# Optimization experiments

Measured on AMD Instinct MI355X. Metric: run time of the kernel, lower is better.

Reference implementation:

```python
import jax, jax.numpy as jnp
import numpy as np

B, T, C = 4, 2048, 768
H, D = 12, 64          # num_heads, head_size
R = 64                 # kv_lora_rank
ROPE_THETA = 10000.0


def setup_inputs() -> dict:
    key = jax.random.key(0)
    ks = jax.random.split(key, 8)
    s = lambda fan_in: 1.0 / np.sqrt(fan_in)
    return {
        "x":      jax.random.normal(ks[0], (B, T, C), jnp.float32),
        "Wq":     jax.random.normal(ks[1], (C, H * D), jnp.float32) * s(C),
        "Wdown":  jax.random.normal(ks[2], (C, R), jnp.float32) * s(C),
        "ln_g":   jnp.ones((R,), jnp.float32),
        "ln_b":   jnp.zeros((R,), jnp.float32),
        "Wup":    jax.random.normal(ks[3], (R, 2 * H * D), jnp.float32) * s(R),
        "Wo":     jax.random.normal(ks[4], (H * D, C), jnp.float32) * s(H * D),
        "bo":     jnp.zeros((C,), jnp.float32),
    }


def _rope_cos_sin(t, d, dtype):
    # freqs over half-dim, repeated twice (rotate-half convention)
    inv_freq = 1.0 / (ROPE_THETA ** (jnp.arange(0, d, 2, dtype=jnp.float32) / d))
    ang = jnp.arange(t, dtype=jnp.float32)[:, None] * inv_freq[None, :]  # [T, D/2]
    ang = jnp.concatenate([ang, ang], axis=-1)                            # [T, D]
    return jnp.cos(ang).astype(dtype), jnp.sin(ang).astype(dtype)


def _apply_rope(q, cos, sin):
    # q: [B, H, T, D]; cos/sin: [T, D]
    d2 = q.shape[-1] // 2
    rot = jnp.concatenate([-q[..., d2:], q[..., :d2]], axis=-1)
    return q * cos + rot * sin


def reference(x, Wq, Wdown, ln_g, ln_b, Wup, Wo, bo):
    b, t, c = x.shape
    q = (x @ Wq).reshape(b, t, H, D).transpose(0, 2, 1, 3)  # [B,H,T,D]

    ckv = x @ Wdown                                         # [B,T,R]
    mu = jnp.mean(ckv, axis=-1, keepdims=True)
    var = jnp.var(ckv, axis=-1, keepdims=True)
    ckv = (ckv - mu) * jax.lax.rsqrt(var + 1e-5) * ln_g + ln_b

    kv = (ckv @ Wup).reshape(b, t, 2, H, D)
    k = kv[:, :, 0].transpose(0, 2, 1, 3)                   # [B,H,T,D]
    v = kv[:, :, 1].transpose(0, 2, 1, 3)

    cos, sin = _rope_cos_sin(t, D, x.dtype)
    q = _apply_rope(q, cos, sin)
    k = _apply_rope(k, cos, sin)

    wei = jnp.einsum("bhqd,bhkd->bhqk", q, k) * (D ** -0.5)
    causal = jnp.tril(jnp.ones((t, t), bool))
    wei = jnp.where(causal, wei, -jnp.inf)
    wei = jax.nn.softmax(wei, axis=-1)                      # dropout: eval mode (identity)

    out = jnp.einsum("bhqk,bhkd->bhqd", wei, v)             # [B,H,T,D]
    out = out.transpose(0, 2, 1, 3).reshape(b, t, H * D)
    return out @ Wo + bo
```

## Files before the change

kernel.cpp:

```cpp
#include <hip/hip_runtime.h>
#include <hip/hip_bf16.h>
#include <math.h>

#define B_ 4
#define T_ 2048
#define C_ 768
#define H_ 12
#define D_ 64
#define R_ 64
#define BT_ (B_*T_)
#define HD_ (H_*D_)

typedef __attribute__((ext_vector_type(8))) short bf16x8;
typedef __attribute__((ext_vector_type(4))) float f32x4;

__device__ inline short f2bf(float f) {
  union { float f; unsigned u; } x; x.f = f;
  unsigned r = x.u + 0x7fffu + ((x.u >> 16) & 1u);
  return (short)(r >> 16);
}
__device__ inline float bf2f(short s) {
  union { unsigned u; float f; } x; x.u = ((unsigned)(unsigned short)s) << 16;
  return x.f;
}
__device__ inline unsigned pk_bf16(float a, float b) {
#if __has_builtin(__builtin_amdgcn_cvt_pk_bf16_f32)
  auto t = __builtin_amdgcn_cvt_pk_bf16_f32(a, b);
  unsigned u; __builtin_memcpy(&u, &t, sizeof(unsigned)); return u;
#else
  union { float f; unsigned u; } x, y; x.f = a; y.f = b;
  unsigned ra = (x.u + 0x7fffu + ((x.u >> 16) & 1u)) >> 16;
  unsigned rb = (y.u + 0x7fffu + ((y.u >> 16) & 1u)) & 0xffff0000u;
  return ra | rb;
#endif
}
__device__ inline float fexp2(float x) {
#if __has_builtin(__builtin_amdgcn_exp2f)
  return __builtin_amdgcn_exp2f(x);
#else
  return exp2f(x);
#endif
}
typedef __attribute__((address_space(3))) unsigned lds_u32;
typedef __attribute__((address_space(1))) const unsigned glb_u32;
__device__ inline void gload_lds16(const void* g, void* l) {
  __builtin_amdgcn_global_load_lds((glb_u32*)g, (lds_u32*)l, 16, 0, 0);
}

__global__ void convert_f32_bf16(const float* __restrict__ in, short* __restrict__ out, int n4) {
  int i = blockIdx.x * blockDim.x + threadIdx.x;
  if (i < n4) {
    float4 v = ((const float4*)in)[i];
    short4 o;
    o.x = f2bf(v.x); o.y = f2bf(v.y); o.z = f2bf(v.z); o.w = f2bf(v.w);
    ((short4*)out)[i] = o;
  }
}

__global__ void transpose_all(const float* __restrict__ Wq, const float* __restrict__ Wd,
                              const float* __restrict__ Wup, const float* __restrict__ Wo,
                              short* __restrict__ W1T, short* __restrict__ WupT,
                              short* __restrict__ WoT) {
  int idx = blockIdx.x * blockDim.x + threadIdx.x;
  const int S1 = 768*768, S2 = 64*768, S3 = 1536*64, S4 = 768*768;
  if (idx < S1) {
    int n = idx / 768, k = idx - n*768;
    W1T[idx] = f2bf(Wq[(size_t)k*768 + n]);
  } else if (idx < S1+S2) {
    int i = idx - S1; int n = i / 768, k = i - n*768;
    W1T[idx] = f2bf(Wd[(size_t)k*64 + n]);
  } else if (idx < S1+S2+S3) {
    int i = idx - S1 - S2; int n = i / 64, k = i - n*64;
    WupT[i] = f2bf(Wup[(size_t)k*1536 + n]);
  } else if (idx < S1+S2+S3+S4) {
    int i = idx - S1 - S2 - S3; int n = i / 768, k = i - n*768;
    WoT[i] = f2bf(Wo[(size_t)k*768 + n]);
  }
}

__global__ void rope_tab(float* __restrict__ cs, float* __restrict__ sn) {
  int idx = blockIdx.x * blockDim.x + threadIdx.x;
  if (idx >= T_ * 32) return;
  int j = idx & 31, t = idx >> 5;
  float invf = exp2f(-(float)j * (13.287712379549449f / 32.f));
  float a = (float)t * invf;
  cs[idx] = cosf(a);
  sn[idx] = sinf(a);
}

template<int MODE>
__global__ __launch_bounds__(256) void gemm128(
    const short* __restrict__ A, const short* __restrict__ Bt,
    int M, int N, int K, int NBvalid,
    float* __restrict__ out0, const float* __restrict__ bias,
    short* __restrict__ ob0, short* __restrict__ ob1,
    const float* __restrict__ cs, const float* __restrict__ sn)
{
  __shared__ short As[128 * 64];
  __shared__ short Bs[128 * 64];
  const int m0 = blockIdx.x * 128;
  const int n0 = blockIdx.y * 128;
  const int tid = threadIdx.x, lane = tid & 63, w = tid >> 6;
  const int wr = w >> 1, wc = w & 1;
  const int fr = lane & 15, fk = (lane >> 4) * 8;
  const int rstage = lane >> 3;
  const int cstage = (lane & 7) * 8;

  f32x4 acc[4][4] = {};

  for (int k0 = 0; k0 < K; k0 += 64) {
    __syncthreads();
    #pragma unroll
    for (int i = 0; i < 4; ++i) {
      int c = w * 4 + i;
      int r = c * 8 + rstage;
      gload_lds16(&A[(size_t)(m0 + r) * K + k0 + cstage], &As[c * 512]);
      if (n0 + c * 8 < NBvalid)
        gload_lds16(&Bt[(size_t)(n0 + r) * K + k0 + cstage], &Bs[c * 512]);
    }
    __syncthreads();
    #pragma unroll
    for (int kk = 0; kk < 64; kk += 32) {
      bf16x8 a[4], b[4];
      #pragma unroll
      for (int i = 0; i < 4; ++i) {
        a[i] = *(const bf16x8*)&As[(wr * 64 + i * 16 + fr) * 64 + kk + fk];
        b[i] = *(const bf16x8*)&Bs[(wc * 64 + i * 16 + fr) * 64 + kk + fk];
      }
      #pragma unroll
      for (int mi = 0; mi < 4; ++mi)
        #pragma unroll
        for (int ni = 0; ni < 4; ++ni)
          acc[mi][ni] = __builtin_amdgcn_mfma_f32_16x16x32_bf16(a[mi], b[ni], acc[mi][ni], 0, 0, 0);
    }
  }

  const int er = (lane >> 4) * 4, ec = lane & 15;
  const int colbase = n0 + wc * 64;

  if constexpr (MODE == 2) {
    #pragma unroll
    for (int mi = 0; mi < 4; ++mi)
      #pragma unroll
      for (int r = 0; r < 4; ++r) {
        int row = m0 + wr * 64 + mi * 16 + er + r;
        #pragma unroll
        for (int ni = 0; ni < 4; ++ni) {
          int col = colbase + ni * 16 + ec;
          out0[(size_t)row * N + col] = acc[mi][ni][r] + bias[col];
        }
      }
    return;
  }

  if (colbase < 768) {
    int h = colbase >> 6;
    #pragma unroll
    for (int mi = 0; mi < 4; ++mi)
      #pragma unroll
      for (int r = 0; r < 4; ++r) {
        int row = m0 + wr * 64 + mi * 16 + er + r;
        int t = row & (T_ - 1), bb = row >> 11;
        short* dst = ob0 + (((size_t)(bb * H_ + h)) * T_ + t) * 64;
        #pragma unroll
        for (int ni = 0; ni < 2; ++ni) {
          int d = ni * 16 + ec;
          float c = cs[t * 32 + d], s = sn[t * 32 + d];
          float x0 = acc[mi][ni][r], x1 = acc[mi][ni + 2][r];
          dst[d]      = f2bf(x0 * c - x1 * s);
          dst[d + 32] = f2bf(x1 * c + x0 * s);
        }
      }
  } else if constexpr (MODE == 0) {
    if (colbase < 832) {
      #pragma unroll
      for (int mi = 0; mi < 4; ++mi)
        #pragma unroll
        for (int r = 0; r < 4; ++r) {
          int row = m0 + wr * 64 + mi * 16 + er + r;
          #pragma unroll
          for (int ni = 0; ni < 4; ++ni)
            ob1[(size_t)row * 64 + ni * 16 + ec] = f2bf(acc[mi][ni][r]);
        }
    }
  } else {
    int h = (colbase - 768) >> 6;
    #pragma unroll
    for (int mi = 0; mi < 4; ++mi) {
      int row0 = m0 + wr * 64 + mi * 16 + er;
      int t = row0 & (T_ - 1), bb = row0 >> 11;
      #pragma unroll
      for (int ni = 0; ni < 4; ++ni) {
        int dd = ni * 16 + ec;
        short4 s4;
        s4.x = f2bf(acc[mi][ni][0]); s4.y = f2bf(acc[mi][ni][1]);
        s4.z = f2bf(acc[mi][ni][2]); s4.w = f2bf(acc[mi][ni][3]);
        *(short4*)&ob1[((size_t)(bb * H_ + h) * 64 + dd) * T_ + t] = s4;
      }
    }
  }
}

__global__ __launch_bounds__(256) void ln_rows(const short* __restrict__ raw,
                                               short* __restrict__ outb,
                                               const float* __restrict__ g,
                                               const float* __restrict__ bta) {
  int row = blockIdx.x * 4 + (threadIdx.x >> 6);
  int lane = threadIdx.x & 63;
  float v = bf2f(raw[(size_t)row * 64 + lane]);
  float s = v, s2 = v * v;
  #pragma unroll
  for (int off = 1; off < 64; off <<= 1) {
    s += __shfl_xor(s, off);
    s2 += __shfl_xor(s2, off);
  }
  float mu = s * (1.f/64.f);
  float var = s2 * (1.f/64.f) - mu * mu;
  float rstd = rsqrtf(var + 1e-5f);
  outb[(size_t)row * 64 + lane] = f2bf((v - mu) * rstd * g[lane] + bta[lane]);
}

#define SC2_ 0.18033688f

__global__ __launch_bounds__(256, 4) void attn_mfma(
    const short* __restrict__ qgl, const short* __restrict__ kg,
    const short* __restrict__ vtg, short* __restrict__ o)
{
  __shared__ short Ks[8 * 512];
  __shared__ short Vts[8 * 512];
  __shared__ short Ps[4 * 32 * 72];

  const int bh = blockIdx.x;
  const int qt = 15 - blockIdx.y;
  const int tid = threadIdx.x, lane = tid & 63, w = tid >> 6;
  const int q16 = lane & 15, quad = lane >> 4;
  const int q0 = qt * 128;
  const int qw = q0 + w * 32;
  short* Pw = &Ps[w * 32 * 72];

  bf16x8 bq[2][2];
  #pragma unroll
  for (int qg = 0; qg < 2; ++qg) {
    const short* qrow = qgl + ((size_t)bh * T_ + qw + qg * 16 + q16) * 64;
    bq[qg][0] = *(const bf16x8*)&qrow[quad * 8];
    bq[qg][1] = *(const bf16x8*)&qrow[32 + quad * 8];
  }
  f32x4 oacc[2][4] = {};
  float lrun[2] = {0.f, 0.f};
  const short* kb  = kg  + (size_t)bh * T_ * 64;
  const short* vtb = vtg + (size_t)bh * 64 * T_;
  const int ktmax = q0 + 64;

  for (int kt = 0; kt <= ktmax; kt += 64) {
    __syncthreads();
    #pragma unroll
    for (int i = 0; i < 2; ++i) {
      int c = w * 2 + i;
      int s = c >> 1, ch = c & 1;
      gload_lds16(kb  + (size_t)(kt + s * 16 + q16) * 64 + ch * 32 + quad * 8, &Ks[c * 512]);
      gload_lds16(vtb + (size_t)(s * 16 + q16) * T_ + kt + ch * 32 + quad * 8, &Vts[c * 512]);
    }
    __syncthreads();

    #pragma unroll
    for (int qg = 0; qg < 2; ++qg) {
      const int qbase = qw + qg * 16;
      if (kt > qbase + 15) continue;
      const bool part = (kt + 63 > qbase);
      float ls = 0.f;
      #pragma unroll
      for (int s = 0; s < 4; ++s) {
        bf16x8 a0 = *(const bf16x8*)&Ks[(s * 2 + 0) * 512 + lane * 8];
        bf16x8 a1 = *(const bf16x8*)&Ks[(s * 2 + 1) * 512 + lane * 8];
        f32x4 t0 = {};
        t0 = __builtin_amdgcn_mfma_f32_16x16x32_bf16(a0, bq[qg][0], t0, 0, 0, 0);
        t0 = __builtin_amdgcn_mfma_f32_16x16x32_bf16(a1, bq[qg][1], t0, 0, 0, 0);
        float pv[4];
        if (!part) {
          #pragma unroll
          for (int r = 0; r < 4; ++r) pv[r] = fexp2(t0[r] * SC2_);
        } else {
          #pragma unroll
          for (int r = 0; r < 4; ++r) {
            int key = kt + s * 16 + quad * 4 + r;
            pv[r] = (key <= qbase + q16) ? fexp2(t0[r] * SC2_) : 0.f;
          }
        }
        ls += (pv[0] + pv[1]) + (pv[2] + pv[3]);
        uint2 uu;
        uu.x = pk_bf16(pv[0], pv[1]);
        uu.y = pk_bf16(pv[2], pv[3]);
        *(uint2*)&Pw[(qg * 16 + q16) * 72 + s * 16 + quad * 4] = uu;
      }
      ls += __shfl_xor(ls, 16);
      ls += __shfl_xor(ls, 32);
      lrun[qg] += ls;

      #pragma unroll
      for (int c = 0; c < 2; ++c) {
        bf16x8 bp = *(const bf16x8*)&Pw[(qg * 16 + q16) * 72 + c * 32 + quad * 8];
        #pragma unroll
        for (int ms = 0; ms < 4; ++ms) {
          bf16x8 av = *(const bf16x8*)&Vts[(ms * 2 + c) * 512 + lane * 8];
          oacc[qg][ms] = __builtin_amdgcn_mfma_f32_16x16x32_bf16(av, bp, oacc[qg][ms], 0, 0, 0);
        }
      }
    }
  }

  int b = bh / H_, h = bh - b * H_;
  #pragma unroll
  for (int qg = 0; qg < 2; ++qg) {
    float inv = 1.f / lrun[qg];
    #pragma unroll
    for (int ms = 0; ms < 4; ++ms) {
      uint2 uu;
      uu.x = pk_bf16(oacc[qg][ms][0] * inv, oacc[qg][ms][1] * inv);
      uu.y = pk_bf16(oacc[qg][ms][2] * inv, oacc[qg][ms][3] * inv);
      *(uint2*)&Pw[(qg * 16 + q16) * 72 + ms * 16 + quad * 4] = uu;
    }
    int row = lane >> 2, cc2 = (lane & 3) * 16;
    uint4 r0 = *(const uint4*)&Pw[(qg * 16 + row) * 72 + cc2];
    uint4 r1 = *(const uint4*)&Pw[(qg * 16 + row) * 72 + cc2 + 8];
    int t = qw + qg * 16 + row;
    short* orow = o + ((size_t)(b * T_ + t)) * HD_ + h * 64 + cc2;
    *(uint4*)&orow[0] = r0;
    *(uint4*)&orow[8] = r1;
  }
}

extern "C" void kernel_launch(void* const* d_in, const int* in_sizes, int n_in,
                              void* d_out, int out_size, void* d_ws, size_t ws_size,
                              hipStream_t stream) {
  (void)in_sizes; (void)n_in; (void)out_size; (void)ws_size;
  const float* x     = (const float*)d_in[0];
  const float* Wq    = (const float*)d_in[1];
  const float* Wdown = (const float*)d_in[2];
  const float* ln_g  = (const float*)d_in[3];
  const float* ln_b  = (const float*)d_in[4];
  const float* Wup   = (const float*)d_in[5];
  const float* Wo    = (const float*)d_in[6];
  const float* bo    = (const float*)d_in[7];
  float* out = (float*)d_out;

  char* w = (char*)d_ws;
  short* x_bf   = (short*)w;  w += (size_t)BT_ * C_    * 2;
  short* W1T    = (short*)w;  w += (size_t)832 * C_    * 2;
  short* WupT   = (short*)w;  w += (size_t)2*HD_ * R_  * 2;
  short* WoT    = (short*)w;  w += (size_t)HD_ * C_    * 2;
  short* ckvraw = (short*)w;  w += (size_t)BT_ * R_    * 2;
  short* ckv    = (short*)w;  w += (size_t)BT_ * R_    * 2;
  short* qb     = (short*)w;  w += (size_t)BT_ * HD_   * 2;
  short* kb     = (short*)w;  w += (size_t)BT_ * HD_   * 2;
  short* vt     = (short*)w;  w += (size_t)BT_ * HD_   * 2;
  short* att    = (short*)w;  w += (size_t)BT_ * HD_   * 2;
  float* cs_t   = (float*)w;  w += (size_t)T_ * 32 * 4;
  float* sn_t   = (float*)w;  w += (size_t)T_ * 32 * 4;

  rope_tab<<<(T_*32 + 255)/256, 256, 0, stream>>>(cs_t, sn_t);
  convert_f32_bf16<<<(BT_*C_/4 + 255)/256, 256, 0, stream>>>(x, x_bf, BT_*C_/4);
  {
    const int tot = 768*768 + 64*768 + 1536*64 + 768*768;
    transpose_all<<<(tot + 255)/256, 256, 0, stream>>>(Wq, Wdown, Wup, Wo, W1T, WupT, WoT);
  }

  gemm128<0><<<dim3(BT_/128, 7), 256, 0, stream>>>(
      x_bf, W1T, BT_, 896, C_, 832, nullptr, nullptr, qb, ckvraw, cs_t, sn_t);

  ln_rows<<<BT_/4, 256, 0, stream>>>(ckvraw, ckv, ln_g, ln_b);

  gemm128<1><<<dim3(BT_/128, 12), 256, 0, stream>>>(
      ckv, WupT, BT_, 2*HD_, R_, 2*HD_, nullptr, nullptr, kb, vt, cs_t, sn_t);

  attn_mfma<<<dim3(B_*H_, T_/128), 256, 0, stream>>>(qb, kb, vt, att);

  gemm128<2><<<dim3(BT_/128, 6), 256, 0, stream>>>(
      att, WoT, BT_, C_, HD_, C_, out, bo, nullptr, nullptr, nullptr, nullptr);
}
```

Measured before the change: 230.3 us.

## Fuse LayerNorm into GEMM epilogue, merge prep kernels, rebalance causal attention tiles

Folds the rope table computation into the weight transpose kernel and fuses the latent LayerNorm into the first GEMM's epilogue, which removes two launches and the round trip through the raw ckv buffer. The V-transpose epilogue now stages through LDS so that global stores are coalesced 16-byte rows. The attention kernel now uses 64-row query tiles with one 16-row group per wave. Each block processes a late tile and its mirrored early tile, balancing causal work across blocks, and the occupancy launch-bound hint is dropped. In exchange, each attention block does more sequential work and has fewer rows per wave to reuse each K/V load.

```diff
diff --git a/kernel.cpp b/kernel.cpp
--- a/kernel.cpp
+++ b/kernel.cpp
@@ -57,12 +57,13 @@
   }
 }
 
-__global__ void transpose_all(const float* __restrict__ Wq, const float* __restrict__ Wd,
-                              const float* __restrict__ Wup, const float* __restrict__ Wo,
-                              short* __restrict__ W1T, short* __restrict__ WupT,
-                              short* __restrict__ WoT) {
+__global__ void prep_all(const float* __restrict__ Wq, const float* __restrict__ Wd,
+                         const float* __restrict__ Wup, const float* __restrict__ Wo,
+                         short* __restrict__ W1T, short* __restrict__ WupT,
+                         short* __restrict__ WoT,
+                         float* __restrict__ cs, float* __restrict__ sn) {
   int idx = blockIdx.x * blockDim.x + threadIdx.x;
-  const int S1 = 768*768, S2 = 64*768, S3 = 1536*64, S4 = 768*768;
+  const int S1 = 768*768, S2 = 64*768, S3 = 1536*64, S4 = 768*768, S5 = T_*32;
   if (idx < S1) {
     int n = idx / 768, k = idx - n*768;
     W1T[idx] = f2bf(Wq[(size_t)k*768 + n]);
@@ -75,17 +76,14 @@
   } else if (idx < S1+S2+S3+S4) {
     int i = idx - S1 - S2 - S3; int n = i / 768, k = i - n*768;
     WoT[i] = f2bf(Wo[(size_t)k*768 + n]);
-  }
-}
-
-__global__ void rope_tab(float* __restrict__ cs, float* __restrict__ sn) {
-  int idx = blockIdx.x * blockDim.x + threadIdx.x;
-  if (idx >= T_ * 32) return;
-  int j = idx & 31, t = idx >> 5;
-  float invf = exp2f(-(float)j * (13.287712379549449f / 32.f));
-  float a = (float)t * invf;
-  cs[idx] = cosf(a);
-  sn[idx] = sinf(a);
+  } else if (idx < S1+S2+S3+S4+S5) {
+    int i = idx - S1 - S2 - S3 - S4;
+    int j = i & 31, t = i >> 5;
+    float invf = exp2f(-(float)j * (13.287712379549449f / 32.f));
+    float a = (float)t * invf;
+    cs[i] = cosf(a);
+    sn[i] = sinf(a);
+  }
 }
 
 template<int MODE>
@@ -93,6 +91,7 @@
     const short* __restrict__ A, const short* __restrict__ Bt,
     int M, int N, int K, int NBvalid,
     float* __restrict__ out0, const float* __restrict__ bias,
+    const float* __restrict__ bias2,
     short* __restrict__ ob0, short* __restrict__ ob1,
     const float* __restrict__ cs, const float* __restrict__ sn)
 {
@@ -153,176 +152,209 @@
     return;
   }
 
-  if (colbase < 768) {
-    int h = colbase >> 6;
-    #pragma unroll
-    for (int mi = 0; mi < 4; ++mi)
-      #pragma unroll
-      for (int r = 0; r < 4; ++r) {
-        int row = m0 + wr * 64 + mi * 16 + er + r;
-        int t = row & (T_ - 1), bb = row >> 11;
-        short* dst = ob0 + (((size_t)(bb * H_ + h)) * T_ + t) * 64;
-        #pragma unroll
-        for (int ni = 0; ni < 2; ++ni) {
-          int d = ni * 16 + ec;
-          float c = cs[t * 32 + d], s = sn[t * 32 + d];
-          float x0 = acc[mi][ni][r], x1 = acc[mi][ni + 2][r];
-          dst[d]      = f2bf(x0 * c - x1 * s);
-          dst[d + 32] = f2bf(x1 * c + x0 * s);
-        }
-      }
-  } else if constexpr (MODE == 0) {
-    if (colbase < 832) {
+  if constexpr (MODE == 0) {
+    if (colbase < 768) {
+      int h = colbase >> 6;
       #pragma unroll
       for (int mi = 0; mi < 4; ++mi)
         #pragma unroll
         for (int r = 0; r < 4; ++r) {
           int row = m0 + wr * 64 + mi * 16 + er + r;
-          #pragma unroll
-          for (int ni = 0; ni < 4; ++ni)
-            ob1[(size_t)row * 64 + ni * 16 + ec] = f2bf(acc[mi][ni][r]);
+          int t = row & (T_ - 1), bb = row >> 11;
+          short* dst = ob0 + (((size_t)(bb * H_ + h)) * T_ + t) * 64;
+          #pragma unroll
+          for (int ni = 0; ni < 2; ++ni) {
+            int d = ni * 16 + ec;
+            float c = cs[t * 32 + d], s = sn[t * 32 + d];
+            float x0 = acc[mi][ni][r], x1 = acc[mi][ni + 2][r];
+            dst[d]      = f2bf(x0 * c - x1 * s);
+            dst[d + 32] = f2bf(x1 * c + x0 * s);
+          }
+        }
+    } else if (colbase < 832) {
+      #pragma unroll
+      for (int mi = 0; mi < 4; ++mi)
+        #pragma unroll
+        for (int r = 0; r < 4; ++r) {
+          float s = 0.f, s2 = 0.f;
+          #pragma unroll
+          for (int ni = 0; ni < 4; ++ni) { float v = acc[mi][ni][r]; s += v; s2 += v*v; }
+          #pragma unroll
+          for (int off = 1; off < 16; off <<= 1) {
+            s  += __shfl_xor(s, off);
+            s2 += __shfl_xor(s2, off);
+          }
+          float mu = s * (1.f/64.f);
+          float var = s2 * (1.f/64.f) - mu * mu;
+          float rstd = rsqrtf(var + 1e-5f);
+          int row = m0 + wr * 64 + mi * 16 + er + r;
+          #pragma unroll
+          for (int ni = 0; ni < 4; ++ni) {
+            int d = ni * 16 + ec;
+            ob1[(size_t)row * 64 + d] = f2bf((acc[mi][ni][r] - mu) * rstd * bias[d] + bias2[d]);
+          }
         }
     }
   } else {
-    int h = (colbase - 768) >> 6;
-    #pragma unroll
-    for (int mi = 0; mi < 4; ++mi) {
-      int row0 = m0 + wr * 64 + mi * 16 + er;
-      int t = row0 & (T_ - 1), bb = row0 >> 11;
-      #pragma unroll
-      for (int ni = 0; ni < 4; ++ni) {
-        int dd = ni * 16 + ec;
-        short4 s4;
-        s4.x = f2bf(acc[mi][ni][0]); s4.y = f2bf(acc[mi][ni][1]);
-        s4.z = f2bf(acc[mi][ni][2]); s4.w = f2bf(acc[mi][ni][3]);
-        *(short4*)&ob1[((size_t)(bb * H_ + h) * 64 + dd) * T_ + t] = s4;
-      }
-    }
-  }
-}
-
-__global__ __launch_bounds__(256) void ln_rows(const short* __restrict__ raw,
-                                               short* __restrict__ outb,
-                                               const float* __restrict__ g,
-                                               const float* __restrict__ bta) {
-  int row = blockIdx.x * 4 + (threadIdx.x >> 6);
-  int lane = threadIdx.x & 63;
-  float v = bf2f(raw[(size_t)row * 64 + lane]);
-  float s = v, s2 = v * v;
-  #pragma unroll
-  for (int off = 1; off < 64; off <<= 1) {
-    s += __shfl_xor(s, off);
-    s2 += __shfl_xor(s2, off);
-  }
-  float mu = s * (1.f/64.f);
-  float var = s2 * (1.f/64.f) - mu * mu;
-  float rstd = rsqrtf(var + 1e-5f);
-  outb[(size_t)row * 64 + lane] = f2bf((v - mu) * rstd * g[lane] + bta[lane]);
+    if (colbase < 768) {
+      int h = colbase >> 6;
+      #pragma unroll
+      for (int mi = 0; mi < 4; ++mi)
+        #pragma unroll
+        for (int r = 0; r < 4; ++r) {
+          int row = m0 + wr * 64 + mi * 16 + er + r;
+          int t = row & (T_ - 1), bb = row >> 11;
+          short* dst = ob0 + (((size_t)(bb * H_ + h)) * T_ + t) * 64;
+          #pragma unroll
+          for (int ni = 0; ni < 2; ++ni) {
+            int d = ni * 16 + ec;
+            float c = cs[t * 32 + d], s = sn[t * 32 + d];
+            float x0 = acc[mi][ni][r], x1 = acc[mi][ni + 2][r];
+            dst[d]      = f2bf(x0 * c - x1 * s);
+            dst[d + 32] = f2bf(x1 * c + x0 * s);
+          }
+        }
+    } else {
+      __syncthreads();
+      short* Wl = (w < 2) ? &As[w * 4096] : &Bs[(w - 2) * 4096];
+      int h = (colbase - 768) >> 6;
+      #pragma unroll
+      for (int mi = 0; mi < 4; ++mi) {
+        int tl0 = mi * 16 + er;
+        #pragma unroll
+        for (int ni = 0; ni < 4; ++ni) {
+          int d = ni * 16 + ec;
+          int col = (tl0 + (d & 7) * 8) & 63;
+          uint2 uu;
+          uu.x = pk_bf16(acc[mi][ni][0], acc[mi][ni][1]);
+          uu.y = pk_bf16(acc[mi][ni][2], acc[mi][ni][3]);
+          *(uint2*)&Wl[d * 64 + col] = uu;
+        }
+      }
+      __syncthreads();
+      int bb = m0 >> 11;
+      int tg0 = (m0 & (T_ - 1)) + wr * 64;
+      int dlow = lane >> 3, tc = lane & 7;
+      #pragma unroll
+      for (int j = 0; j < 8; ++j) {
+        int d = j * 8 + dlow;
+        int col = (tc * 8 + (d & 7) * 8) & 63;
+        uint4 vv = *(const uint4*)&Wl[d * 64 + col];
+        *(uint4*)&ob1[((size_t)(bb * H_ + h) * 64 + d) * T_ + tg0 + tc * 8] = vv;
+      }
+    }
+  }
 }
 
 #define SC2_ 0.18033688f
 
-__global__ __launch_bounds__(256, 4) void attn_mfma(
+__global__ __launch_bounds__(256) void attn_mfma(
     const short* __restrict__ qgl, const short* __restrict__ kg,
     const short* __restrict__ vtg, short* __restrict__ o)
 {
   __shared__ short Ks[8 * 512];
   __shared__ short Vts[8 * 512];
-  __shared__ short Ps[4 * 32 * 72];
+  __shared__ short Ps[4 * 16 * 72];
 
   const int bh = blockIdx.x;
-  const int qt = 15 - blockIdx.y;
   const int tid = threadIdx.x, lane = tid & 63, w = tid >> 6;
   const int q16 = lane & 15, quad = lane >> 4;
-  const int q0 = qt * 128;
-  const int qw = q0 + w * 32;
-  short* Pw = &Ps[w * 32 * 72];
-
-  bf16x8 bq[2][2];
-  #pragma unroll
-  for (int qg = 0; qg < 2; ++qg) {
-    const short* qrow = qgl + ((size_t)bh * T_ + qw + qg * 16 + q16) * 64;
-    bq[qg][0] = *(const bf16x8*)&qrow[quad * 8];
-    bq[qg][1] = *(const bf16x8*)&qrow[32 + quad * 8];
-  }
-  f32x4 oacc[2][4] = {};
-  float lrun[2] = {0.f, 0.f};
+  short* Pw = &Ps[w * 16 * 72];
   const short* kb  = kg  + (size_t)bh * T_ * 64;
   const short* vtb = vtg + (size_t)bh * 64 * T_;
-  const int ktmax = q0 + 64;
-
-  for (int kt = 0; kt <= ktmax; kt += 64) {
-    __syncthreads();
-    #pragma unroll
-    for (int i = 0; i < 2; ++i) {
-      int c = w * 2 + i;
-      int s = c >> 1, ch = c & 1;
-      gload_lds16(kb  + (size_t)(kt + s * 16 + q16) * 64 + ch * 32 + quad * 8, &Ks[c * 512]);
-      gload_lds16(vtb + (size_t)(s * 16 + q16) * T_ + kt + ch * 32 + quad * 8, &Vts[c * 512]);
-    }
-    __syncthreads();
-
-    #pragma unroll
-    for (int qg = 0; qg < 2; ++qg) {
-      const int qbase = qw + qg * 16;
-      if (kt > qbase + 15) continue;
-      const bool part = (kt + 63 > qbase);
-      float ls = 0.f;
+  const int b = bh / H_, h = bh - b * H_;
+
+  #pragma unroll
+  for (int phase = 0; phase < 2; ++phase) {
+    const int qt = phase == 0 ? (31 - (int)blockIdx.y) : (int)blockIdx.y;
+    const int q0 = qt * 64 + w * 16;
+    const int qidx = q0 + q16;
+
+    const short* qrow = qgl + ((size_t)bh * T_ + qidx) * 64;
+    bf16x8 bq0 = *(const bf16x8*)&qrow[quad * 8];
+    bf16x8 bq1 = *(const bf16x8*)&qrow[32 + quad * 8];
+
+    f32x4 oacc[4] = {};
+    float lrun = 0.f;
+    const int qlast = qt * 64;
+
+    for (int kt = 0; kt <= qlast; kt += 64) {
+      __syncthreads();
+      #pragma unroll
+      for (int i = 0; i < 2; ++i) {
+        int c = w * 2 + i;
+        int s = c >> 1, ch = c & 1;
+        gload_lds16(kb  + (size_t)(kt + s * 16 + q16) * 64 + ch * 32 + quad * 8, &Ks[c * 512]);
+        gload_lds16(vtb + (size_t)(s * 16 + q16) * T_ + kt + ch * 32 + quad * 8, &Vts[c * 512]);
+      }
+      __syncthreads();
+
+      f32x4 sacc[4];
       #pragma unroll
       for (int s = 0; s < 4; ++s) {
         bf16x8 a0 = *(const bf16x8*)&Ks[(s * 2 + 0) * 512 + lane * 8];
         bf16x8 a1 = *(const bf16x8*)&Ks[(s * 2 + 1) * 512 + lane * 8];
         f32x4 t0 = {};
-        t0 = __builtin_amdgcn_mfma_f32_16x16x32_bf16(a0, bq[qg][0], t0, 0, 0, 0);
-        t0 = __builtin_amdgcn_mfma_f32_16x16x32_bf16(a1, bq[qg][1], t0, 0, 0, 0);
-        float pv[4];
-        if (!part) {
-          #pragma unroll
-          for (int r = 0; r < 4; ++r) pv[r] = fexp2(t0[r] * SC2_);
-        } else {
+        t0 = __builtin_amdgcn_mfma_f32_16x16x32_bf16(a0, bq0, t0, 0, 0, 0);
+        t0 = __builtin_amdgcn_mfma_f32_16x16x32_bf16(a1, bq1, t0, 0, 0, 0);
+        sacc[s] = t0;
+      }
+
+      float pv[16];
+      float ls = 0.f;
+      if (kt != qlast) {
+        #pragma unroll
+        for (int s = 0; s < 4; ++s)
+          #pragma unroll
+          for (int r = 0; r < 4; ++r) {
+            float p = fexp2(sacc[s][r] * SC2_);
+            pv[s * 4 + r] = p; ls += p;
+          }
+      } else {
+        #pragma unroll
+        for (int s = 0; s < 4; ++s)
           #pragma unroll
           for (int r = 0; r < 4; ++r) {
             int key = kt + s * 16 + quad * 4 + r;
-            pv[r] = (key <= qbase + q16) ? fexp2(t0[r] * SC2_) : 0.f;
-          }
-        }
-        ls += (pv[0] + pv[1]) + (pv[2] + pv[3]);
-        uint2 uu;
-        uu.x = pk_bf16(pv[0], pv[1]);
-        uu.y = pk_bf16(pv[2], pv[3]);
-        *(uint2*)&Pw[(qg * 16 + q16) * 72 + s * 16 + quad * 4] = uu;
+            float p = (key <= qidx) ? fexp2(sacc[s][r] * SC2_) : 0.f;
+            pv[s * 4 + r] = p; ls += p;
+          }
       }
       ls += __shfl_xor(ls, 16);
       ls += __shfl_xor(ls, 32);
-      lrun[qg] += ls;
+      lrun += ls;
+
+      #pragma unroll
+      for (int s = 0; s < 4; ++s) {
+        uint2 uu;
+        uu.x = pk_bf16(pv[s * 4 + 0], pv[s * 4 + 1]);
+        uu.y = pk_bf16(pv[s * 4 + 2], pv[s * 4 + 3]);
+        *(uint2*)&Pw[q16 * 72 + s * 16 + quad * 4] = uu;
+      }
 
       #pragma unroll
       for (int c = 0; c < 2; ++c) {
-        bf16x8 bp = *(const bf16x8*)&Pw[(qg * 16 + q16) * 72 + c * 32 + quad * 8];
+        bf16x8 bp = *(const bf16x8*)&Pw[q16 * 72 + c * 32 + quad * 8];
         #pragma unroll
         for (int ms = 0; ms < 4; ++ms) {
           bf16x8 av = *(const bf16x8*)&Vts[(ms * 2 + c) * 512 + lane * 8];
-          oacc[qg][ms] = __builtin_amdgcn_mfma_f32_16x16x32_bf16(av, bp, oacc[qg][ms], 0, 0, 0);
-        }
-      }
-    }
-  }
-
-  int b = bh / H_, h = bh - b * H_;
-  #pragma unroll
-  for (int qg = 0; qg < 2; ++qg) {
-    float inv = 1.f / lrun[qg];
+          oacc[ms] = __builtin_amdgcn_mfma_f32_16x16x32_bf16(av, bp, oacc[ms], 0, 0, 0);
+        }
+      }
+    }
+
+    float inv = 1.f / lrun;
     #pragma unroll
     for (int ms = 0; ms < 4; ++ms) {
       uint2 uu;
-      uu.x = pk_bf16(oacc[qg][ms][0] * inv, oacc[qg][ms][1] * inv);
-      uu.y = pk_bf16(oacc[qg][ms][2] * inv, oacc[qg][ms][3] * inv);
-      *(uint2*)&Pw[(qg * 16 + q16) * 72 + ms * 16 + quad * 4] = uu;
+      uu.x = pk_bf16(oacc[ms][0] * inv, oacc[ms][1] * inv);
+      uu.y = pk_bf16(oacc[ms][2] * inv, oacc[ms][3] * inv);
+      *(uint2*)&Pw[q16 * 72 + ms * 16 + quad * 4] = uu;
     }
     int row = lane >> 2, cc2 = (lane & 3) * 16;
-    uint4 r0 = *(const uint4*)&Pw[(qg * 16 + row) * 72 + cc2];
-    uint4 r1 = *(const uint4*)&Pw[(qg * 16 + row) * 72 + cc2 + 8];
-    int t = qw + qg * 16 + row;
+    uint4 r0 = *(const uint4*)&Pw[row * 72 + cc2];
+    uint4 r1 = *(const uint4*)&Pw[row * 72 + cc2 + 8];
+    int t = q0 + row;
     short* orow = o + ((size_t)(b * T_ + t)) * HD_ + h * 64 + cc2;
     *(uint4*)&orow[0] = r0;
     *(uint4*)&orow[8] = r1;
@@ -348,7 +380,6 @@
   short* W1T    = (short*)w;  w += (size_t)832 * C_    * 2;
   short* WupT   = (short*)w;  w += (size_t)2*HD_ * R_  * 2;
   short* WoT    = (short*)w;  w += (size_t)HD_ * C_    * 2;
-  short* ckvraw = (short*)w;  w += (size_t)BT_ * R_    * 2;
   short* ckv    = (short*)w;  w += (size_t)BT_ * R_    * 2;
   short* qb     = (short*)w;  w += (size_t)BT_ * HD_   * 2;
   short* kb     = (short*)w;  w += (size_t)BT_ * HD_   * 2;
@@ -357,23 +388,20 @@
   float* cs_t   = (float*)w;  w += (size_t)T_ * 32 * 4;
   float* sn_t   = (float*)w;  w += (size_t)T_ * 32 * 4;
 
-  rope_tab<<<(T_*32 + 255)/256, 256, 0, stream>>>(cs_t, sn_t);
+  {
+    const int tot = 768*768 + 64*768 + 1536*64 + 768*768 + T_*32;
+    prep_all<<<(tot + 255)/256, 256, 0, stream>>>(Wq, Wdown, Wup, Wo, W1T, WupT, WoT, cs_t, sn_t);
+  }
   convert_f32_bf16<<<(BT_*C_/4 + 255)/256, 256, 0, stream>>>(x, x_bf, BT_*C_/4);
-  {
-    const int tot = 768*768 + 64*768 + 1536*64 + 768*768;
-    transpose_all<<<(tot + 255)/256, 256, 0, stream>>>(Wq, Wdown, Wup, Wo, W1T, WupT, WoT);
-  }
 
   gemm128<0><<<dim3(BT_/128, 7), 256, 0, stream>>>(
-      x_bf, W1T, BT_, 896, C_, 832, nullptr, nullptr, qb, ckvraw, cs_t, sn_t);
-
-  ln_rows<<<BT_/4, 256, 0, stream>>>(ckvraw, ckv, ln_g, ln_b);
+      x_bf, W1T, BT_, 896, C_, 832, nullptr, ln_g, ln_b, qb, ckv, cs_t, sn_t);
 
   gemm128<1><<<dim3(BT_/128, 12), 256, 0, stream>>>(
-      ckv, WupT, BT_, 2*HD_, R_, 2*HD_, nullptr, nullptr, kb, vt, cs_t, sn_t);
-
-  attn_mfma<<<dim3(B_*H_, T_/128), 256, 0, stream>>>(qb, kb, vt, att);
+      ckv, WupT, BT_, 2*HD_, R_, 2*HD_, nullptr, nullptr, nullptr, kb, vt, cs_t, sn_t);
+
+  attn_mfma<<<dim3(B_*H_, 16), 256, 0, stream>>>(qb, kb, vt, att);
 
   gemm128<2><<<dim3(BT_/128, 6), 256, 0, stream>>>(
-      att, WoT, BT_, C_, HD_, C_, out, bo, nullptr, nullptr, nullptr, nullptr);
-}
+      att, WoT, BT_, C_, HD_, C_, out, bo, nullptr, nullptr, nullptr, nullptr, nullptr);
+}
```

Result: faster. 207.2 us (-10.0%).
